# Kernel optimization log

Hardware: AMD Instinct MI355X
Metric: run time of the kernel (lower is better)

## Reference

```python
import jax, jax.numpy as jnp
import numpy as np

B, T, E, H = 2, 2048, 1024, 16
HS = E // H  # head size = 64
EPS = 1e-5


def setup_inputs() -> dict:
    key = jax.random.key(0)
    ks = jax.random.split(key, 12)
    s_e = 1.0 / np.sqrt(E)
    s_4e = 1.0 / np.sqrt(4 * E)
    return {
        "x": jax.random.normal(ks[0], (B, T, E), dtype=jnp.float32),
        # per-head projections (no bias), stacked over heads: [H, E, HS]
        "Wq": jax.random.uniform(ks[1], (H, E, HS), jnp.float32, -s_e, s_e),
        "Wk": jax.random.uniform(ks[2], (H, E, HS), jnp.float32, -s_e, s_e),
        "Wv": jax.random.uniform(ks[3], (H, E, HS), jnp.float32, -s_e, s_e),
        # output projection
        "Wo": jax.random.uniform(ks[4], (E, E), jnp.float32, -s_e, s_e),
        "bo": jax.random.uniform(ks[5], (E,), jnp.float32, -s_e, s_e),
        # feed-forward
        "W1": jax.random.uniform(ks[6], (E, 4 * E), jnp.float32, -s_e, s_e),
        "b1": jax.random.uniform(ks[7], (4 * E,), jnp.float32, -s_e, s_e),
        "W2": jax.random.uniform(ks[8], (4 * E, E), jnp.float32, -s_4e, s_4e),
        "b2": jax.random.uniform(ks[9], (E,), jnp.float32, -s_4e, s_4e),
        # layernorms
        "g1": jnp.ones((E,), jnp.float32),
        "be1": jnp.zeros((E,), jnp.float32),
        "g2": jnp.ones((E,), jnp.float32),
        "be2": jnp.zeros((E,), jnp.float32),
    }


def _layernorm(x, g, b):
    mu = jnp.mean(x, axis=-1, keepdims=True)
    var = jnp.var(x, axis=-1, keepdims=True)
    return (x - mu) * jax.lax.rsqrt(var + EPS) * g + b


def reference(x, Wq, Wk, Wv, Wo, bo, W1, b1, W2, b2, g1, be1, g2, be2):
    Bx, Tx, Ex = x.shape
    # --- multi-head causal self-attention (dropout = identity in eval) ---
    q = jnp.einsum("bte,hed->bhtd", x, Wq)
    k = jnp.einsum("bte,hed->bhtd", x, Wk)
    v = jnp.einsum("bte,hed->bhtd", x, Wv)
    scale = HS ** -0.5
    scores = jnp.einsum("bhtd,bhsd->bhts", q, k) * scale  # [B,H,T,T]
    causal = jnp.tril(jnp.ones((Tx, Tx), dtype=bool))
    scores = jnp.where(causal, scores, -jnp.inf)
    att = jax.nn.softmax(scores, axis=-1)
    out = jnp.einsum("bhts,bhsd->bhtd", att, v)  # [B,H,T,HS]
    out = out.transpose(0, 2, 1, 3).reshape(Bx, Tx, Ex)  # concat heads
    out = out @ Wo + bo
    # --- residual + LN1 ---
    x = _layernorm(x + out, g1, be1)
    # --- feed-forward ---
    h = jax.nn.relu(x @ W1 + b1)
    ff = h @ W2 + b2
    # --- residual + LN2 ---
    return _layernorm(x + ff, g2, be2)
```

## Files before the change

### kernel.cpp

```cpp
#include <hip/hip_runtime.h>
#include <hip/hip_bf16.h>
#include <cstdint>
#include <cstddef>

typedef __hip_bfloat16 bf16;
typedef __attribute__((ext_vector_type(8))) short short8;
typedef __attribute__((ext_vector_type(4))) float f32x4;

#define B_  2
#define T_  2048
#define E_  1024
#define H_  16
#define HS_ 64
#define EPS_ 1e-5f
#define NEG_BIG -1.0e30f
#define SCL2E 0.18033688011112042f

__device__ __forceinline__ float b2f(bf16 v) { return __bfloat162float(v); }
__device__ __forceinline__ bf16  f2b(float v) { return __float2bfloat16(v); }
__device__ __forceinline__ ushort f2bs(float v) { bf16 b = __float2bfloat16(v); return *(ushort*)&b; }
__device__ __forceinline__ float ld1(const bf16* p) { return b2f(*p); }
__device__ __forceinline__ float ld1(const float* p) { return *p; }
__device__ __forceinline__ void st1(bf16* p, float v) { *p = f2b(v); }
__device__ __forceinline__ void st1(float* p, float v) { *p = v; }

__device__ __forceinline__ float fexp2(float x) {
#if __has_builtin(__builtin_amdgcn_exp2f)
    return __builtin_amdgcn_exp2f(x);
#else
    return exp2f(x);
#endif
}

__device__ __forceinline__ void gload16(const void* g, const void* l) {
    __builtin_amdgcn_global_load_lds(
        (const __attribute__((address_space(1))) unsigned int*)(size_t)g,
        (__attribute__((address_space(3))) unsigned int*)(unsigned int)(size_t)l,
        16, 0, 0);
}

__device__ __forceinline__ void transpose_tile_s(short t[64][72],
                                                 const float* in, size_t ldin,
                                                 bf16* out, size_t ldout,
                                                 int r0, int c0)
{
    const int tid = threadIdx.x;
    const int tr = tid >> 2, tc4 = (tid & 3) * 16;

    const float* p = in + (size_t)(r0 + tr) * ldin + c0 + tc4;
    float4 v0 = ((const float4*)p)[0], v1 = ((const float4*)p)[1];
    float4 v2 = ((const float4*)p)[2], v3 = ((const float4*)p)[3];
    union { ushort u[16]; uint4 q[2]; } pk;
    pk.u[0] = f2bs(v0.x); pk.u[1] = f2bs(v0.y); pk.u[2]  = f2bs(v0.z); pk.u[3]  = f2bs(v0.w);
    pk.u[4] = f2bs(v1.x); pk.u[5] = f2bs(v1.y); pk.u[6]  = f2bs(v1.z); pk.u[7]  = f2bs(v1.w);
    pk.u[8] = f2bs(v2.x); pk.u[9] = f2bs(v2.y); pk.u[10] = f2bs(v2.z); pk.u[11] = f2bs(v2.w);
    pk.u[12] = f2bs(v3.x); pk.u[13] = f2bs(v3.y); pk.u[14] = f2bs(v3.z); pk.u[15] = f2bs(v3.w);
    *(uint4*)&t[tr][tc4]     = pk.q[0];
    *(uint4*)&t[tr][tc4 + 8] = pk.q[1];
    __syncthreads();

    const int tcI = tid >> 2, rj = (tid & 3) * 16;
    union { ushort u[16]; uint4 q[2]; } po;
    #pragma unroll
    for (int j = 0; j < 16; j++) po.u[j] = (ushort)t[rj + j][tcI];
    bf16* op = out + (size_t)(c0 + tcI) * ldout + r0 + rj;
    ((uint4*)op)[0] = po.q[0];
    ((uint4*)op)[1] = po.q[1];
}

__global__ __launch_bounds__(256) void prep_kernel(const float* __restrict__ x,
                                                   ushort* __restrict__ xb,
                                                   const float* __restrict__ Wq,
                                                   const float* __restrict__ Wk,
                                                   const float* __restrict__ Wv,
                                                   bf16* __restrict__ WqkvT,
                                                   const float* __restrict__ Wo,
                                                   bf16* __restrict__ WoT)
{
    __shared__ short t[64][72];
    const int bid = blockIdx.x;
    if (bid < 2048) {
        int i = (bid * 256 + (int)threadIdx.x) * 8;
        float4 a = ((const float4*)(x + i))[0];
        float4 b = ((const float4*)(x + i))[1];
        union { ushort u[8]; uint4 v; } p;
        p.u[0] = f2bs(a.x); p.u[1] = f2bs(a.y); p.u[2] = f2bs(a.z); p.u[3] = f2bs(a.w);
        p.u[4] = f2bs(b.x); p.u[5] = f2bs(b.y); p.u[6] = f2bs(b.z); p.u[7] = f2bs(b.w);
        *(uint4*)(xb + i) = p.v;
    } else if (bid < 2048 + 768) {
        const int i = bid - 2048;
        const int s = i >> 4, xt = i & 15;
        const int proj = s >> 4, h = s & 15;
        const float* W = (proj == 0) ? Wq : ((proj == 1) ? Wk : Wv);
        transpose_tile_s(t, W + (size_t)h * E_ * HS_, HS_,
                         WqkvT + ((size_t)proj * E_ + h * 64) * E_, E_,
                         xt * 64, 0);
    } else {
        const int i = bid - 2816;
        transpose_tile_s(t, Wo, E_, WoT, E_, (i >> 4) * 64, (i & 15) * 64);
    }
}

__global__ __launch_bounds__(256) void prep2_kernel(const float* __restrict__ W1,
                                                    bf16* __restrict__ W1T,
                                                    const float* __restrict__ W2,
                                                    bf16* __restrict__ W2T)
{
    __shared__ short t[64][72];
    const int bid = blockIdx.x;
    if (bid < 1024) {
        transpose_tile_s(t, W1, 4 * E_, W1T, E_,
                         (bid & 15) * 64, (bid >> 4) * 64);
    } else {
        const int i = bid - 1024;
        transpose_tile_s(t, W2, E_, W2T, 4 * E_,
                         (i >> 4) * 64, (i & 15) * 64);
    }
}

__global__ __launch_bounds__(256) void vt_transpose(const bf16* __restrict__ qkv,
                                                    bf16* __restrict__ vT)
{
    __shared__ short t[64][72];
    const int tid = threadIdx.x;
    const int bh  = blockIdx.y;
    const int b   = bh >> 4, h = bh & 15;
    const int t0  = blockIdx.x * 64;

    const bf16* in = qkv + ((size_t)b * T_) * (3 * E_) + 2 * E_ + h * 64;
    const int tr = tid >> 2, tc4 = (tid & 3) * 16;
    const bf16* p = in + (size_t)(t0 + tr) * (3 * E_) + tc4;
    uint4 q0 = ((const uint4*)p)[0];
    uint4 q1 = ((const uint4*)p)[1];
    *(uint4*)&t[tr][tc4]     = q0;
    *(uint4*)&t[tr][tc4 + 8] = q1;
    __syncthreads();

    const int tcI = tid >> 2, rj = (tid & 3) * 16;
    union { ushort u[16]; uint4 q[2]; } po;
    #pragma unroll
    for (int j = 0; j < 16; j++) po.u[j] = (ushort)t[rj + j][tcI];
    bf16* op = vT + ((size_t)bh * 64 + tcI) * T_ + t0 + rj;
    ((uint4*)op)[0] = po.q[0];
    ((uint4*)op)[1] = po.q[1];
}

template <int WROWS, int WCOLS, int MF, int NF, int KS, bool BIAS, bool RELU,
          typename TO>
__global__ __launch_bounds__(256) void gemm_bt(const bf16* __restrict__ A,
                                               const bf16* __restrict__ BT,
                                               const float* __restrict__ bias,
                                               TO* __restrict__ C,
                                               int M, int N, int K)
{
    constexpr int BM = WROWS * MF * 16;
    constexpr int BN = WCOLS * NF * 16;
    __shared__ short Asm[KS][BM][32];
    __shared__ short Bsm[KS][BN][32];

    const int tid  = threadIdx.x;
    const int wv   = tid >> 6, lane = tid & 63;
    const int quad = lane >> 4, l16 = lane & 15;
    const int row0 = blockIdx.y * BM, col0 = blockIdx.x * BN;
    const int mr0  = (wv / WCOLS) * MF * 16;
    const int nc0  = (wv % WCOLS) * NF * 16;

    const int sr = tid >> 2, sc = tid & 3;
    const bf16* Ag = A  + (size_t)(row0 + sr) * K + sc * 8;
    const bf16* Bg = BT + (size_t)(col0 + (sr % BN)) * K + sc * 8;

    f32x4 acc[MF][NF];
    #pragma unroll
    for (int i = 0; i < MF; i++)
        #pragma unroll
        for (int j = 0; j < NF; j++) acc[i][j] = (f32x4){0.f, 0.f, 0.f, 0.f};

    for (int kt = 0; kt < K; kt += 32 * KS) {
        __syncthreads();
        #pragma unroll
        for (int g = 0; g < KS; g++) {
            #pragma unroll
            for (int l = 0; l < BM / 64; l++)
                gload16(Ag + g * 32 + (size_t)l * 64 * K, &Asm[g][l * 64 + wv * 16][0]);
            #pragma unroll
            for (int l = 0; l < BN / 64; l++)
                gload16(Bg + g * 32 + (size_t)l * 64 * K, &Bsm[g][l * 64 + wv * 16][0]);
        }
        Ag += 32 * KS; Bg += 32 * KS;
        __syncthreads();

        #pragma unroll
        for (int g = 0; g < KS; g++) {
            short8 af[MF], bfr[NF];
            #pragma unroll
            for (int mf = 0; mf < MF; mf++)
                af[mf] = *(const short8*)&Asm[g][mr0 + mf * 16 + l16][quad * 8];
            #pragma unroll
            for (int nf = 0; nf < NF; nf++)
                bfr[nf] = *(const short8*)&Bsm[g][nc0 + nf * 16 + l16][quad * 8];
            #pragma unroll
            for (int mf = 0; mf < MF; mf++)
                #pragma unroll
                for (int nf = 0; nf < NF; nf++)
                    acc[mf][nf] = __builtin_amdgcn_mfma_f32_16x16x32_bf16(
                        af[mf], bfr[nf], acc[mf][nf], 0, 0, 0);
        }
    }

    #pragma unroll
    for (int nf = 0; nf < NF; nf++) {
        const int col = col0 + nc0 + nf * 16 + l16;
        const float bv = BIAS ? bias[col] : 0.f;
        #pragma unroll
        for (int mf = 0; mf < MF; mf++) {
            #pragma unroll
            for (int r = 0; r < 4; r++) {
                const int row = row0 + mr0 + mf * 16 + quad * 4 + r;
                float v = acc[mf][nf][r] + bv;
                if (RELU) v = fmaxf(v, 0.f);
                st1(&C[(size_t)row * N + col], v);
            }
        }
    }
}

__global__ __launch_bounds__(256) void attn_mfma(const bf16* __restrict__ qkv,
                                                 const bf16* __restrict__ vT,
                                                 bf16* __restrict__ outp)
{
    __shared__ short Klds[128][72];
    __shared__ short Vlds[64][136];
    __shared__ short Plds[4][16][136];

    const int tid  = threadIdx.x;
    const int w    = tid >> 6, lane = tid & 63;
    const int quad = lane >> 4, l16 = lane & 15;

    const int p    = blockIdx.y * 32 + blockIdx.x;
    const int bh   = (p & 7) * 4 + ((p >> 3) & 3);
    const int tile = 31 - (p >> 5);
    const int b    = bh >> 4, h = bh & 15;
    const size_t rowb = (size_t)b * T_ * 3 * E_;
    const int t0    = tile * 64;
    const int qbase = t0 + w * 16;

    const int kkey = tid >> 1, kdh = (tid & 1) * 32;
    const bf16* Kg = qkv + rowb + E_ + h * HS_ + kdh;
    const int vd = tid >> 2, vseg = (tid & 3) * 32;
    const bf16* Vg = vT + ((size_t)bh * 64 + vd) * T_;

    const bf16* Qp = qkv + rowb + (size_t)(qbase + l16) * (3 * E_) + h * HS_;
    const short8 aq0 = *(const short8*)(Qp + quad * 8);
    const short8 aq1 = *(const short8*)(Qp + 32 + quad * 8);

    short8 vone;
    #pragma unroll
    for (int j = 0; j < 8; j++) vone[j] = (short)0x3F80;

    f32x4 o[4], o4;
    #pragma unroll
    for (int f = 0; f < 4; f++) o[f] = (f32x4){0.f, 0.f, 0.f, 0.f};
    o4 = (f32x4){0.f, 0.f, 0.f, 0.f};
    float mrow = NEG_BIG;

    for (int kt0 = 0; kt0 <= t0; kt0 += 128) {
        uint4 kq[4], vq[4];
        {
            const int krr = kt0 + kkey;
            const int kr = (krr < T_) ? krr : T_ - 1;
            const bf16* kp = Kg + (size_t)kr * (3 * E_);
            #pragma unroll
            for (int i = 0; i < 4; i++) kq[i] = ((const uint4*)kp)[i];
            #pragma unroll
            for (int i = 0; i < 4; i++) {
                int col = kt0 + vseg + i * 8;
                col = (col < T_ - 8) ? col : T_ - 8;
                vq[i] = *(const uint4*)(Vg + col);
            }
        }
        __syncthreads();
        #pragma unroll
        for (int i = 0; i < 4; i++) *(uint4*)&Klds[kkey][kdh + i * 8] = kq[i];
        #pragma unroll
        for (int i = 0; i < 4; i++) *(uint4*)&Vlds[vd][vseg + i * 8] = vq[i];
        __syncthreads();

        const int nv0 = ((qbase + 15 - kt0) >> 4) + 1;
        const int nvalid = nv0 < 8 ? nv0 : 8;

        float ps[8][4];
        #pragma unroll
        for (int c = 0; c < 8; c++) {
            if (c < nvalid) {
                const int krow = c * 16 + l16;
                short8 bk0 = *(const short8*)&Klds[krow][quad * 8];
                short8 bk1 = *(const short8*)&Klds[krow][32 + quad * 8];
                f32x4 s = (f32x4){0.f, 0.f, 0.f, 0.f};
                s = __builtin_amdgcn_mfma_f32_16x16x32_bf16(bk0, aq0, s, 0, 0, 0);
                s = __builtin_amdgcn_mfma_f32_16x16x32_bf16(bk1, aq1, s, 0, 0, 0);
                const int kc = kt0 + c * 16;
                const bool needmask = (kc + 15 > qbase);
                #pragma unroll
                for (int r = 0; r < 4; r++) {
                    float sv = s[r] * SCL2E;
                    if (needmask && (kc + quad * 4 + r > qbase + l16)) sv = NEG_BIG;
                    ps[c][r] = sv;
                }
            }
        }

        float mx = ps[0][0];
        #pragma unroll
        for (int r = 1; r < 4; r++) mx = fmaxf(mx, ps[0][r]);
        #pragma unroll
        for (int c = 1; c < 8; c++)
            if (c < nvalid)
                #pragma unroll
                for (int r = 0; r < 4; r++) mx = fmaxf(mx, ps[c][r]);
        mx = fmaxf(mx, __shfl_xor(mx, 16));
        mx = fmaxf(mx, __shfl_xor(mx, 32));
        const float mnew = fmaxf(mrow, mx);
        const float al = fexp2(mrow - mnew);
        mrow = mnew;

        #pragma unroll
        for (int c = 0; c < 8; c++) {
            uint2 pk; pk.x = 0u; pk.y = 0u;
            if (c < nvalid) {
                const float e0 = fexp2(ps[c][0] - mnew);
                const float e1 = fexp2(ps[c][1] - mnew);
                const float e2 = fexp2(ps[c][2] - mnew);
                const float e3 = fexp2(ps[c][3] - mnew);
                pk.x = (uint)f2bs(e0) | ((uint)f2bs(e1) << 16);
                pk.y = (uint)f2bs(e2) | ((uint)f2bs(e3) << 16);
            }
            *(uint2*)&Plds[w][l16][c * 16 + quad * 4] = pk;
        }

        float alo[4];
        #pragma unroll
        for (int r = 0; r < 4; r++) alo[r] = __shfl(al, quad * 4 + r);
        #pragma unroll
        for (int f = 0; f < 4; f++)
            #pragma unroll
            for (int r = 0; r < 4; r++) o[f][r] *= alo[r];
        #pragma unroll
        for (int r = 0; r < 4; r++) o4[r] *= alo[r];

        __builtin_amdgcn_s_setprio(1);
        #pragma unroll
        for (int kg = 0; kg < 4; kg++) {
            short8 pa = *(const short8*)&Plds[w][l16][kg * 32 + quad * 8];
            #pragma unroll
            for (int f = 0; f < 4; f++) {
                short8 vb = *(const short8*)&Vlds[f * 16 + l16][kg * 32 + quad * 8];
                o[f] = __builtin_amdgcn_mfma_f32_16x16x32_bf16(pa, vb, o[f], 0, 0, 0);
            }
            o4 = __builtin_amdgcn_mfma_f32_16x16x32_bf16(pa, vone, o4, 0, 0, 0);
        }
        __builtin_amdgcn_s_setprio(0);
    }

    #pragma unroll
    for (int r = 0; r < 4; r++) {
        const float linv = 1.f / o4[r];
        bf16* op = outp + (size_t)(b * T_ + qbase + quad * 4 + r) * E_ + h * HS_;
        #pragma unroll
        for (int f = 0; f < 4; f++)
            op[f * 16 + l16] = f2b(o[f][r] * linv);
    }
}

template <typename TA, typename TR, typename TO>
__global__ __launch_bounds__(256) void ln_kernel(const TA* a,
                                                 const TR* r,
                                                 const float* g,
                                                 const float* be,
                                                 TO* out)
{
    const int row = blockIdx.x;
    const TA* pa = a + (size_t)row * E_;
    const TR* pr = r + (size_t)row * E_;
    TO* po = out + (size_t)row * E_;

    float v[4];
    float sum = 0.f, sq = 0.f;
    #pragma unroll
    for (int j = 0; j < 4; j++) {
        int c = threadIdx.x + j * 256;
        v[j] = ld1(pa + c) + ld1(pr + c);
        sum += v[j];
        sq  += v[j] * v[j];
    }
    #pragma unroll
    for (int o = 32; o >= 1; o >>= 1) {
        sum += __shfl_xor(sum, o);
        sq  += __shfl_xor(sq, o);
    }
    __shared__ float red[8];
    const int wave = threadIdx.x >> 6, lane = threadIdx.x & 63;
    if (lane == 0) { red[wave] = sum; red[4 + wave] = sq; }
    __syncthreads();
    sum = red[0] + red[1] + red[2] + red[3];
    sq  = red[4] + red[5] + red[6] + red[7];

    const float mu  = sum * (1.f / E_);
    const float var = fmaxf(sq * (1.f / E_) - mu * mu, 0.f);
    const float rs  = rsqrtf(var + EPS_);

    #pragma unroll
    for (int j = 0; j < 4; j++) {
        int c = threadIdx.x + j * 256;
        st1(po + c, (v[j] - mu) * rs * g[c] + be[c]);
    }
}

extern "C" void kernel_launch(void* const* d_in, const int* in_sizes, int n_in,
                              void* d_out, int out_size, void* d_ws, size_t ws_size,
                              hipStream_t stream)
{
    (void)in_sizes; (void)n_in; (void)out_size; (void)ws_size;
    const float* x   = (const float*)d_in[0];
    const float* Wq  = (const float*)d_in[1];
    const float* Wk  = (const float*)d_in[2];
    const float* Wv  = (const float*)d_in[3];
    const float* Wo  = (const float*)d_in[4];
    const float* bo  = (const float*)d_in[5];
    const float* W1  = (const float*)d_in[6];
    const float* b1  = (const float*)d_in[7];
    const float* W2  = (const float*)d_in[8];
    const float* b2  = (const float*)d_in[9];
    const float* g1  = (const float*)d_in[10];
    const float* be1 = (const float*)d_in[11];
    const float* g2  = (const float*)d_in[12];
    const float* be2 = (const float*)d_in[13];

    const int M = B_ * T_;
    char* ws = (char*)d_ws;
    bf16* WqkvT = (bf16*)(ws);
    bf16* qkv   = (bf16*)(ws + (size_t)6291456);
    bf16* WoT   = (bf16*)(ws + (size_t)31457280);
    bf16* W1T   = (bf16*)(ws);
    bf16* W2T   = (bf16*)(ws + (size_t)8388608);
    bf16* proj  = (bf16*)(ws + (size_t)16777216);
    bf16* y     = (bf16*)(ws + (size_t)25165824);
    bf16* ff    = (bf16*)(ws + (size_t)16777216);

    bf16*  xb      = (bf16*)d_out;
    bf16*  vT      = (bf16*)d_out;
    bf16*  attnout = (bf16*)((char*)d_out + (size_t)8388608);
    bf16*  hbuf    = (bf16*)d_out;
    float* outf    = (float*)d_out;

    prep_kernel<<<3072, 256, 0, stream>>>(x, (ushort*)xb, Wq, Wk, Wv, WqkvT, Wo, WoT);

    gemm_bt<2, 2, 4, 4, 2, false, false, bf16><<<dim3(24, 32), 256, 0, stream>>>(
        xb, WqkvT, nullptr, qkv, M, 3 * E_, E_);

    vt_transpose<<<dim3(T_ / 64, B_ * H_), 256, 0, stream>>>(qkv, vT);

    attn_mfma<<<dim3(32, 32), 256, 0, stream>>>(qkv, vT, attnout);

    prep2_kernel<<<2048, 256, 0, stream>>>(W1, W1T, W2, W2T);

    gemm_bt<2, 2, 4, 2, 2, true, false, bf16><<<dim3(16, 32), 256, 0, stream>>>(
        attnout, WoT, bo, proj, M, E_, E_);

    ln_kernel<float, bf16, bf16><<<M, 256, 0, stream>>>(x, proj, g1, be1, y);

    for (int half = 0; half < 2; half++) {
        const size_t r0 = (size_t)half * 2048;
        gemm_bt<2, 2, 4, 4, 2, true, true, bf16><<<dim3(32, 16), 256, 0, stream>>>(
            y + r0 * E_, W1T, b1, hbuf, 2048, 4 * E_, E_);
        gemm_bt<2, 2, 2, 2, 2, true, false, bf16><<<dim3(16, 32), 256, 0, stream>>>(
            hbuf, W2T, b2, ff + r0 * E_, 2048, E_, 4 * E_);
    }

    ln_kernel<bf16, bf16, float><<<M, 256, 0, stream>>>(y, ff, g2, be2, outf);
}
```

Baseline: 445.1 us.

## Pair causal query tiles per block to balance attention workload

Each attention block now processes two query tiles, xt and 31-xt, so every block does about the same amount of causal work, and the grid is halved. The K/V loads are now written straight to LDS rather than staged through registers before the barrier, and the s_setprio hints are removed. Waves whose rows are fully masked now skip the softmax and PV work. The trade-offs are half as many blocks in flight and less overlap between global loads and compute.

```diff
diff --git a/kernel.cpp b/kernel.cpp
--- a/kernel.cpp
+++ b/kernel.cpp
@@ -236,138 +236,136 @@
     const int w    = tid >> 6, lane = tid & 63;
     const int quad = lane >> 4, l16 = lane & 15;
 
-    const int p    = blockIdx.y * 32 + blockIdx.x;
+    const int p    = blockIdx.y * 16 + blockIdx.x;
     const int bh   = (p & 7) * 4 + ((p >> 3) & 3);
-    const int tile = 31 - (p >> 5);
+    const int xt   = p >> 5;
     const int b    = bh >> 4, h = bh & 15;
     const size_t rowb = (size_t)b * T_ * 3 * E_;
-    const int t0    = tile * 64;
-    const int qbase = t0 + w * 16;
 
     const int kkey = tid >> 1, kdh = (tid & 1) * 32;
     const bf16* Kg = qkv + rowb + E_ + h * HS_ + kdh;
     const int vd = tid >> 2, vseg = (tid & 3) * 32;
-    const bf16* Vg = vT + ((size_t)bh * 64 + vd) * T_;
-
-    const bf16* Qp = qkv + rowb + (size_t)(qbase + l16) * (3 * E_) + h * HS_;
-    const short8 aq0 = *(const short8*)(Qp + quad * 8);
-    const short8 aq1 = *(const short8*)(Qp + 32 + quad * 8);
+    const bf16* Vg = vT + ((size_t)bh * 64 + vd) * T_ + vseg;
 
     short8 vone;
     #pragma unroll
     for (int j = 0; j < 8; j++) vone[j] = (short)0x3F80;
 
-    f32x4 o[4], o4;
-    #pragma unroll
-    for (int f = 0; f < 4; f++) o[f] = (f32x4){0.f, 0.f, 0.f, 0.f};
-    o4 = (f32x4){0.f, 0.f, 0.f, 0.f};
-    float mrow = NEG_BIG;
-
-    for (int kt0 = 0; kt0 <= t0; kt0 += 128) {
-        uint4 kq[4], vq[4];
-        {
-            const int krr = kt0 + kkey;
-            const int kr = (krr < T_) ? krr : T_ - 1;
-            const bf16* kp = Kg + (size_t)kr * (3 * E_);
-            #pragma unroll
-            for (int i = 0; i < 4; i++) kq[i] = ((const uint4*)kp)[i];
-            #pragma unroll
-            for (int i = 0; i < 4; i++) {
-                int col = kt0 + vseg + i * 8;
-                col = (col < T_ - 8) ? col : T_ - 8;
-                vq[i] = *(const uint4*)(Vg + col);
+    for (int pass = 0; pass < 2; pass++) {
+        const int t0 = (pass == 0 ? xt : 31 - xt) * 64;
+        const int qbase = t0 + w * 16;
+
+        const bf16* Qp = qkv + rowb + (size_t)(qbase + l16) * (3 * E_) + h * HS_;
+        const short8 aq0 = *(const short8*)(Qp + quad * 8);
+        const short8 aq1 = *(const short8*)(Qp + 32 + quad * 8);
+
+        f32x4 o[4], o4;
+        #pragma unroll
+        for (int f = 0; f < 4; f++) o[f] = (f32x4){0.f, 0.f, 0.f, 0.f};
+        o4 = (f32x4){0.f, 0.f, 0.f, 0.f};
+        float mrow = NEG_BIG;
+
+        for (int kt0 = 0; kt0 <= t0; kt0 += 128) {
+            __syncthreads();
+            {
+                const int kr = (kt0 + kkey < T_) ? kt0 + kkey : T_ - 1;
+                const bf16* kp = Kg + (size_t)kr * (3 * E_);
+                *(uint4*)&Klds[kkey][kdh]      = ((const uint4*)kp)[0];
+                *(uint4*)&Klds[kkey][kdh + 8]  = ((const uint4*)kp)[1];
+                *(uint4*)&Klds[kkey][kdh + 16] = ((const uint4*)kp)[2];
+                *(uint4*)&Klds[kkey][kdh + 24] = ((const uint4*)kp)[3];
+                const bf16* vp = Vg + kt0;
+                *(uint4*)&Vlds[vd][vseg]       = ((const uint4*)vp)[0];
+                *(uint4*)&Vlds[vd][vseg + 8]   = ((const uint4*)vp)[1];
+                *(uint4*)&Vlds[vd][vseg + 16]  = ((const uint4*)vp)[2];
+                *(uint4*)&Vlds[vd][vseg + 24]  = ((const uint4*)vp)[3];
             }
-        }
-        __syncthreads();
-        #pragma unroll
-        for (int i = 0; i < 4; i++) *(uint4*)&Klds[kkey][kdh + i * 8] = kq[i];
-        #pragma unroll
-        for (int i = 0; i < 4; i++) *(uint4*)&Vlds[vd][vseg + i * 8] = vq[i];
-        __syncthreads();
-
-        const int nv0 = ((qbase + 15 - kt0) >> 4) + 1;
-        const int nvalid = nv0 < 8 ? nv0 : 8;
-
-        float ps[8][4];
-        #pragma unroll
-        for (int c = 0; c < 8; c++) {
-            if (c < nvalid) {
-                const int krow = c * 16 + l16;
-                short8 bk0 = *(const short8*)&Klds[krow][quad * 8];
-                short8 bk1 = *(const short8*)&Klds[krow][32 + quad * 8];
-                f32x4 s = (f32x4){0.f, 0.f, 0.f, 0.f};
-                s = __builtin_amdgcn_mfma_f32_16x16x32_bf16(bk0, aq0, s, 0, 0, 0);
-                s = __builtin_amdgcn_mfma_f32_16x16x32_bf16(bk1, aq1, s, 0, 0, 0);
-                const int kc = kt0 + c * 16;
-                const bool needmask = (kc + 15 > qbase);
-                #pragma unroll
-                for (int r = 0; r < 4; r++) {
-                    float sv = s[r] * SCL2E;
-                    if (needmask && (kc + quad * 4 + r > qbase + l16)) sv = NEG_BIG;
-                    ps[c][r] = sv;
+            __syncthreads();
+
+            const bool active = (kt0 <= qbase + 15);
+            const int nv0 = ((qbase + 15 - kt0) >> 4) + 1;
+            const int nvalid = active ? (nv0 < 8 ? nv0 : 8) : 0;
+
+            float ps[8][4];
+            #pragma unroll
+            for (int c = 0; c < 8; c++) {
+                if (c < nvalid) {
+                    const int kc = kt0 + c * 16;
+                    const int krow = c * 16 + l16;
+                    short8 bk0 = *(const short8*)&Klds[krow][quad * 8];
+                    short8 bk1 = *(const short8*)&Klds[krow][32 + quad * 8];
+                    f32x4 s = (f32x4){0.f, 0.f, 0.f, 0.f};
+                    s = __builtin_amdgcn_mfma_f32_16x16x32_bf16(bk0, aq0, s, 0, 0, 0);
+                    s = __builtin_amdgcn_mfma_f32_16x16x32_bf16(bk1, aq1, s, 0, 0, 0);
+                    const bool needmask = (kc + 15 > qbase);
+                    #pragma unroll
+                    for (int r = 0; r < 4; r++) {
+                        float sv = s[r] * SCL2E;
+                        if (needmask && (kc + quad * 4 + r > qbase + l16)) sv = NEG_BIG;
+                        ps[c][r] = sv;
+                    }
+                }
+            }
+            if (active) {
+                float mx = ps[0][0];
+                #pragma unroll
+                for (int r = 1; r < 4; r++) mx = fmaxf(mx, ps[0][r]);
+                #pragma unroll
+                for (int c = 1; c < 8; c++)
+                    if (c < nvalid)
+                        #pragma unroll
+                        for (int r = 0; r < 4; r++) mx = fmaxf(mx, ps[c][r]);
+                mx = fmaxf(mx, __shfl_xor(mx, 16));
+                mx = fmaxf(mx, __shfl_xor(mx, 32));
+                const float mnew = fmaxf(mrow, mx);
+                const float al = fexp2(mrow - mnew);
+                mrow = mnew;
+
+                #pragma unroll
+                for (int c = 0; c < 8; c++) {
+                    uint2 pk; pk.x = 0u; pk.y = 0u;
+                    if (c < nvalid) {
+                        const float e0 = fexp2(ps[c][0] - mnew);
+                        const float e1 = fexp2(ps[c][1] - mnew);
+                        const float e2 = fexp2(ps[c][2] - mnew);
+                        const float e3 = fexp2(ps[c][3] - mnew);
+                        pk.x = (uint)f2bs(e0) | ((uint)f2bs(e1) << 16);
+                        pk.y = (uint)f2bs(e2) | ((uint)f2bs(e3) << 16);
+                    }
+                    *(uint2*)&Plds[w][l16][c * 16 + quad * 4] = pk;
+                }
+
+                float alo[4];
+                #pragma unroll
+                for (int r = 0; r < 4; r++) alo[r] = __shfl(al, quad * 4 + r);
+                #pragma unroll
+                for (int f = 0; f < 4; f++)
+                    #pragma unroll
+                    for (int r = 0; r < 4; r++) o[f][r] *= alo[r];
+                #pragma unroll
+                for (int r = 0; r < 4; r++) o4[r] *= alo[r];
+
+                #pragma unroll
+                for (int kg = 0; kg < 4; kg++) {
+                    short8 pa = *(const short8*)&Plds[w][l16][kg * 32 + quad * 8];
+                    #pragma unroll
+                    for (int f = 0; f < 4; f++) {
+                        short8 vb = *(const short8*)&Vlds[f * 16 + l16][kg * 32 + quad * 8];
+                        o[f] = __builtin_amdgcn_mfma_f32_16x16x32_bf16(pa, vb, o[f], 0, 0, 0);
+                    }
+                    o4 = __builtin_amdgcn_mfma_f32_16x16x32_bf16(pa, vone, o4, 0, 0, 0);
                 }
             }
         }
 
-        float mx = ps[0][0];
-        #pragma unroll
-        for (int r = 1; r < 4; r++) mx = fmaxf(mx, ps[0][r]);
-        #pragma unroll
-        for (int c = 1; c < 8; c++)
-            if (c < nvalid)
-                #pragma unroll
-                for (int r = 0; r < 4; r++) mx = fmaxf(mx, ps[c][r]);
-        mx = fmaxf(mx, __shfl_xor(mx, 16));
-        mx = fmaxf(mx, __shfl_xor(mx, 32));
-        const float mnew = fmaxf(mrow, mx);
-        const float al = fexp2(mrow - mnew);
-        mrow = mnew;
-
-        #pragma unroll
-        for (int c = 0; c < 8; c++) {
-            uint2 pk; pk.x = 0u; pk.y = 0u;
-            if (c < nvalid) {
-                const float e0 = fexp2(ps[c][0] - mnew);
-                const float e1 = fexp2(ps[c][1] - mnew);
-                const float e2 = fexp2(ps[c][2] - mnew);
-                const float e3 = fexp2(ps[c][3] - mnew);
-                pk.x = (uint)f2bs(e0) | ((uint)f2bs(e1) << 16);
-                pk.y = (uint)f2bs(e2) | ((uint)f2bs(e3) << 16);
-            }
-            *(uint2*)&Plds[w][l16][c * 16 + quad * 4] = pk;
+        #pragma unroll
+        for (int r = 0; r < 4; r++) {
+            const float linv = 1.f / o4[r];
+            bf16* op = outp + (size_t)(b * T_ + qbase + quad * 4 + r) * E_ + h * HS_;
+            #pragma unroll
+            for (int f = 0; f < 4; f++)
+                op[f * 16 + l16] = f2b(o[f][r] * linv);
         }
-
-        float alo[4];
-        #pragma unroll
-        for (int r = 0; r < 4; r++) alo[r] = __shfl(al, quad * 4 + r);
-        #pragma unroll
-        for (int f = 0; f < 4; f++)
-            #pragma unroll
-            for (int r = 0; r < 4; r++) o[f][r] *= alo[r];
-        #pragma unroll
-        for (int r = 0; r < 4; r++) o4[r] *= alo[r];
-
-        __builtin_amdgcn_s_setprio(1);
-        #pragma unroll
-        for (int kg = 0; kg < 4; kg++) {
-            short8 pa = *(const short8*)&Plds[w][l16][kg * 32 + quad * 8];
-            #pragma unroll
-            for (int f = 0; f < 4; f++) {
-                short8 vb = *(const short8*)&Vlds[f * 16 + l16][kg * 32 + quad * 8];
-                o[f] = __builtin_amdgcn_mfma_f32_16x16x32_bf16(pa, vb, o[f], 0, 0, 0);
-            }
-            o4 = __builtin_amdgcn_mfma_f32_16x16x32_bf16(pa, vone, o4, 0, 0, 0);
-        }
-        __builtin_amdgcn_s_setprio(0);
-    }
-
-    #pragma unroll
-    for (int r = 0; r < 4; r++) {
-        const float linv = 1.f / o4[r];
-        bf16* op = outp + (size_t)(b * T_ + qbase + quad * 4 + r) * E_ + h * HS_;
-        #pragma unroll
-        for (int f = 0; f < 4; f++)
-            op[f * 16 + l16] = f2b(o[f][r] * linv);
     }
 }
 
@@ -459,7 +457,7 @@
 
     vt_transpose<<<dim3(T_ / 64, B_ * H_), 256, 0, stream>>>(qkv, vT);
 
-    attn_mfma<<<dim3(32, 32), 256, 0, stream>>>(qkv, vT, attnout);
+    attn_mfma<<<dim3(16, 32), 256, 0, stream>>>(qkv, vT, attnout);
 
     prep2_kernel<<<2048, 256, 0, stream>>>(W1, W1T, W2, W2T);
 
```

After: 405.7 us. 8.8% less time.
